# Kernel optimization log

Hardware: AMD Instinct MI355X
Metric: run time of the kernel (lower is better)

Reference implementation:

```python
import jax, jax.numpy as jnp
import numpy as np

VOCAB = 65  # 26 + 26 + 10 + 3
EMBED = 6
MAX_CTX = 8192
B, T = 4, 8192


def setup_inputs() -> dict:
    key = jax.random.key(0)
    ks = jax.random.split(key, 8)
    x = jax.random.randint(ks[0], (B, T), 0, VOCAB)
    embed_w = jax.random.normal(ks[1], (VOCAB, EMBED), dtype=jnp.float32)
    # nn.Parameter(torch.tril(torch.rand(...)))
    position_mask = jnp.tril(jax.random.uniform(ks[2], (MAX_CTX, MAX_CTX), dtype=jnp.float32))
    reset_threshold = jax.random.normal(ks[3], (1,), dtype=jnp.float32)
    temperature = jnp.sqrt(jnp.asarray(0.01, dtype=jnp.float32))
    class_transition = jax.random.normal(ks[4], (EMBED, EMBED), dtype=jnp.float32)
    reset_transition = jax.random.normal(ks[5], (EMBED, EMBED), dtype=jnp.float32)
    output = jax.random.normal(ks[6], (EMBED, VOCAB), dtype=jnp.float32)
    return {
        "x": x,
        "embed_w": embed_w,
        "position_mask": position_mask,
        "reset_threshold": reset_threshold,
        "temperature": temperature,
        "class_transition": class_transition,
        "reset_transition": reset_transition,
        "output": output,
    }


def reference(x, embed_w, position_mask, reset_threshold, temperature,
              class_transition, reset_transition, output):
    emb = embed_w[x]                               # [B,T,E]
    class_prob = jax.nn.softmax(emb, axis=-1)      # [B,T,E]
    t = x.shape[1]
    # causal pairwise similarity, weighted and reduced
    sim = jnp.einsum('bte,bse->bts', class_prob, class_prob)   # [B,T,T]
    weights = jnp.tril(position_mask[:t, :t])                  # [T,T]
    score = jnp.sum(sim * weights, axis=-1)                    # [B,T]
    score_scaled = (score - reset_threshold ** 2) / temperature ** 2
    reset = jax.nn.sigmoid(score_scaled)[..., None]            # [B,T,1]
    transition_class = class_prob @ class_transition           # [B,T,E]
    reset_class = class_prob @ reset_transition                # [B,T,E]
    next_class = reset * reset_class + (1.0 - reset) * transition_class
    return next_class @ output                                 # [B,T,V]
```

## Files before the change

### kernel.cpp

```cpp
#include <hip/hip_runtime.h>
#include <cmath>

typedef float f32x4 __attribute__((ext_vector_type(4)));

#define TT 8192
#define NV 65

__device__ __forceinline__ float dot4acc(f32x4 a, f32x4 b, float acc) {
  acc = fmaf(a[0], b[0], acc);
  acc = fmaf(a[1], b[1], acc);
  acc = fmaf(a[2], b[2], acc);
  acc = fmaf(a[3], b[3], acc);
  return acc;
}

__global__ __launch_bounds__(256) void cp_kernel(const int* __restrict__ x,
                                                 const float* __restrict__ ew,
                                                 float* __restrict__ cpt) {
  int n = blockIdx.x * 256 + threadIdx.x;
  int b = n >> 13, t = n & 8191;
  int xv = x[n];
  float v[6];
#pragma unroll
  for (int e = 0; e < 6; ++e) v[e] = ew[xv * 6 + e];
  float m = v[0];
#pragma unroll
  for (int e = 1; e < 6; ++e) m = fmaxf(m, v[e]);
  float s = 0.f;
#pragma unroll
  for (int e = 0; e < 6; ++e) { v[e] = expf(v[e] - m); s += v[e]; }
  float inv = 1.f / s;
#pragma unroll
  for (int e = 0; e < 6; ++e) cpt[(b * 6 + e) * TT + t] = v[e] * inv;
}

__global__ __launch_bounds__(256) void sticky_main(
    const float* __restrict__ W, const float* __restrict__ cpt,
    const float* __restrict__ rtp, const float* __restrict__ tp,
    const float* __restrict__ CT, const float* __restrict__ RT,
    const float* __restrict__ OM, float* __restrict__ out) {
  __shared__ __align__(16) float cp_lds[24][256];
  __shared__ __align__(16) float wsum_lds[4][4][24];
  const int j = blockIdx.x;
  const int tid = threadIdx.x;
  const int w = tid >> 6, lane = tid & 63;
  const int rbase = (w < 2) ? (8 * j + 4 * w) : (8184 - 8 * j + 4 * (w - 2));
  const int wmax = rbase + 3;
  const int k_need = 8192 - 8 * j;
  const int kl = lane * 4;

  float acc[4][24];
#pragma unroll
  for (int r = 0; r < 4; ++r)
#pragma unroll
    for (int e = 0; e < 24; ++e) acc[r][e] = 0.f;

  for (int kc = 0; kc < k_need; kc += 256) {
    __syncthreads();
#pragma unroll
    for (int i = 0; i < 6; ++i) {
      int f = tid + 256 * i;
      int e = f >> 6, c4 = (f & 63) * 4;
      *reinterpret_cast<f32x4*>(&cp_lds[e][c4]) =
          *reinterpret_cast<const f32x4*>(&cpt[e * TT + kc + c4]);
    }
    __syncthreads();
    if (kc <= wmax) {
      const float* wp = &W[(size_t)rbase * TT + kc + kl];
      f32x4 w0 = __builtin_nontemporal_load(reinterpret_cast<const f32x4*>(wp));
      f32x4 w1 = __builtin_nontemporal_load(reinterpret_cast<const f32x4*>(wp + TT));
      f32x4 w2 = __builtin_nontemporal_load(reinterpret_cast<const f32x4*>(wp + 2 * TT));
      f32x4 w3 = __builtin_nontemporal_load(reinterpret_cast<const f32x4*>(wp + 3 * TT));
#pragma unroll
      for (int e = 0; e < 24; ++e) {
        f32x4 c = *reinterpret_cast<const f32x4*>(&cp_lds[e][kl]);
        acc[0][e] = dot4acc(w0, c, acc[0][e]);
        acc[1][e] = dot4acc(w1, c, acc[1][e]);
        acc[2][e] = dot4acc(w2, c, acc[2][e]);
        acc[3][e] = dot4acc(w3, c, acc[3][e]);
      }
    }
  }

#pragma unroll
  for (int r = 0; r < 4; ++r)
#pragma unroll
    for (int e = 0; e < 24; ++e) {
      float v0 = acc[r][e];
      v0 += __shfl_xor(v0, 1);
      v0 += __shfl_xor(v0, 2);
      v0 += __shfl_xor(v0, 4);
      v0 += __shfl_xor(v0, 8);
      v0 += __shfl_xor(v0, 16);
      v0 += __shfl_xor(v0, 32);
      acc[r][e] = v0;
    }
  if (lane == 0) {
#pragma unroll
    for (int r = 0; r < 4; ++r)
#pragma unroll
      for (int g = 0; g < 6; ++g) {
        f32x4 t4;
        t4[0] = acc[r][4 * g + 0];
        t4[1] = acc[r][4 * g + 1];
        t4[2] = acc[r][4 * g + 2];
        t4[3] = acc[r][4 * g + 3];
        *reinterpret_cast<f32x4*>(&wsum_lds[w][r][4 * g]) = t4;
      }
  }
  __syncthreads();

  const int rb = lane & 15;
  const int r = rb >> 2, b = rb & 3, vi = lane >> 4;
  const int t = rbase + r;
  float cp6[6], ws6[6];
#pragma unroll
  for (int e = 0; e < 6; ++e) {
    cp6[e] = cpt[(b * 6 + e) * TT + t];
    ws6[e] = wsum_lds[w][r][b * 6 + e];
  }
  float score = 0.f;
#pragma unroll
  for (int e = 0; e < 6; ++e) score = fmaf(cp6[e], ws6[e], score);
  float rt = rtp[0];
  float temp = tp[0];
  float z = (score - rt * rt) / (temp * temp);
  float reset = 1.f / (1.f + expf(-z));
  float nc[6];
#pragma unroll
  for (int c = 0; c < 6; ++c) {
    float tc = 0.f, rc = 0.f;
#pragma unroll
    for (int e = 0; e < 6; ++e) {
      tc = fmaf(cp6[e], CT[e * 6 + c], tc);
      rc = fmaf(cp6[e], RT[e * 6 + c], rc);
    }
    nc[c] = reset * rc + (1.f - reset) * tc;
  }
  size_t obase = ((size_t)b * TT + t) * NV;
  for (int v = vi; v < NV; v += 4) {
    float o = 0.f;
#pragma unroll
    for (int c = 0; c < 6; ++c) o = fmaf(nc[c], OM[c * NV + v], o);
    out[obase + v] = o;
  }
}

extern "C" void kernel_launch(void* const* d_in, const int* in_sizes, int n_in,
                              void* d_out, int out_size, void* d_ws, size_t ws_size,
                              hipStream_t stream) {
  const int* x = (const int*)d_in[0];
  const float* ew = (const float*)d_in[1];
  const float* W = (const float*)d_in[2];
  const float* rtp = (const float*)d_in[3];
  const float* tp = (const float*)d_in[4];
  const float* CT = (const float*)d_in[5];
  const float* RT = (const float*)d_in[6];
  const float* OM = (const float*)d_in[7];
  float* out = (float*)d_out;
  float* cpt = (float*)d_ws;

  hipLaunchKernelGGL(cp_kernel, dim3(128), dim3(256), 0, stream, x, ew, cpt);
  hipLaunchKernelGGL(sticky_main, dim3(512), dim3(256), 0, stream,
                     W, cpt, rtp, tp, CT, RT, OM, out);
}
```

Baseline: 75.51 us.

## Split-K triangular tiling of weighted similarity with atomic reduction and separate epilogue

The single fused kernel, which walked k-chunks through shared memory, is replaced by a split-K kernel. It enumerates only the lower-triangular 16-row by 1024-column tiles of the position mask, each wave covering 8 rows and 12 of the 24 class columns. Class probabilities are read straight from global memory rather than staged in shared memory, which removes the per-chunk barriers. Partial sums are combined with atomicAdd into a workspace that the class-probability kernel zeroes first. A new elementwise epilogue kernel then computes the output with one thread per output element. The aims are better load balance and more bytes in flight for the large mask read, at the cost of atomics, an extra launch and redundant epilogue math.

New measurement: 113.2 us. 1.5x slower.

```diff
diff --git a/kernel.cpp b/kernel.cpp
--- a/kernel.cpp
+++ b/kernel.cpp
@@ -2,9 +2,13 @@
 #include <cmath>
 
 typedef float f32x4 __attribute__((ext_vector_type(4)));
+typedef float f32x2 __attribute__((ext_vector_type(2)));
 
 #define TT 8192
 #define NV 65
+#define KTILE 1024
+#define SUBK 256
+#define NBLK_B 2304
 
 __device__ __forceinline__ float dot4acc(f32x4 a, f32x4 b, float acc) {
   acc = fmaf(a[0], b[0], acc);
@@ -16,7 +20,8 @@
 
 __global__ __launch_bounds__(256) void cp_kernel(const int* __restrict__ x,
                                                  const float* __restrict__ ew,
-                                                 float* __restrict__ cpt) {
+                                                 float* __restrict__ cpt,
+                                                 float* __restrict__ wsum) {
   int n = blockIdx.x * 256 + threadIdx.x;
   int b = n >> 13, t = n & 8191;
   int xv = x[n];
@@ -32,92 +37,95 @@
   float inv = 1.f / s;
 #pragma unroll
   for (int e = 0; e < 6; ++e) cpt[(b * 6 + e) * TT + t] = v[e] * inv;
+  f32x2 z2 = {0.f, 0.f};
+#pragma unroll
+  for (int i = 0; i < 3; ++i)
+    *reinterpret_cast<f32x2*>(&wsum[6 * n + 2 * i]) = z2;
 }
 
-__global__ __launch_bounds__(256) void sticky_main(
-    const float* __restrict__ W, const float* __restrict__ cpt,
-    const float* __restrict__ rtp, const float* __restrict__ tp,
-    const float* __restrict__ CT, const float* __restrict__ RT,
-    const float* __restrict__ OM, float* __restrict__ out) {
-  __shared__ __align__(16) float cp_lds[24][256];
-  __shared__ __align__(16) float wsum_lds[4][4][24];
-  const int j = blockIdx.x;
+__global__ __launch_bounds__(256, 3) void sticky_B(const float* __restrict__ W,
+                                                   const float* __restrict__ cpt,
+                                                   float* __restrict__ wsum) {
+  __shared__ float ws_lds[16][24];
   const int tid = threadIdx.x;
   const int w = tid >> 6, lane = tid & 63;
-  const int rbase = (w < 2) ? (8 * j + 4 * w) : (8184 - 8 * j + 4 * (w - 2));
-  const int wmax = rbase + 3;
-  const int k_need = 8192 - 8 * j;
-  const int kl = lane * 4;
+  int bid = blockIdx.x;
+  int g = 0;
+#pragma unroll
+  for (int gg = 1; gg < 8; ++gg)
+    if (bid >= 32 * gg * (gg + 1)) g = gg;
+  int rem = bid - 32 * g * (g + 1);
+  int rt = 64 * g + rem / (g + 1);
+  int kt = rem % (g + 1);
+  const int R = rt * 16;
+  const int k0 = kt * KTILE;
+  const int rb = R + 8 * (w >> 1);
+  const int eb = 12 * (w & 1);
 
-  float acc[4][24];
+  float acc[8][12];
 #pragma unroll
-  for (int r = 0; r < 4; ++r)
+  for (int r = 0; r < 8; ++r)
 #pragma unroll
-    for (int e = 0; e < 24; ++e) acc[r][e] = 0.f;
+    for (int e2 = 0; e2 < 12; ++e2) acc[r][e2] = 0.f;
 
-  for (int kc = 0; kc < k_need; kc += 256) {
-    __syncthreads();
+#pragma unroll 1
+  for (int s = 0; s < KTILE / SUBK; ++s) {
+    const int kc = k0 + s * SUBK + lane * 4;
+    const float* wp = &W[(size_t)rb * TT + kc];
+    f32x4 wv[8];
 #pragma unroll
-    for (int i = 0; i < 6; ++i) {
-      int f = tid + 256 * i;
-      int e = f >> 6, c4 = (f & 63) * 4;
-      *reinterpret_cast<f32x4*>(&cp_lds[e][c4]) =
-          *reinterpret_cast<const f32x4*>(&cpt[e * TT + kc + c4]);
-    }
-    __syncthreads();
-    if (kc <= wmax) {
-      const float* wp = &W[(size_t)rbase * TT + kc + kl];
-      f32x4 w0 = __builtin_nontemporal_load(reinterpret_cast<const f32x4*>(wp));
-      f32x4 w1 = __builtin_nontemporal_load(reinterpret_cast<const f32x4*>(wp + TT));
-      f32x4 w2 = __builtin_nontemporal_load(reinterpret_cast<const f32x4*>(wp + 2 * TT));
-      f32x4 w3 = __builtin_nontemporal_load(reinterpret_cast<const f32x4*>(wp + 3 * TT));
+    for (int r = 0; r < 8; ++r)
+      wv[r] = __builtin_nontemporal_load(
+          reinterpret_cast<const f32x4*>(wp + (size_t)r * TT));
 #pragma unroll
-      for (int e = 0; e < 24; ++e) {
-        f32x4 c = *reinterpret_cast<const f32x4*>(&cp_lds[e][kl]);
-        acc[0][e] = dot4acc(w0, c, acc[0][e]);
-        acc[1][e] = dot4acc(w1, c, acc[1][e]);
-        acc[2][e] = dot4acc(w2, c, acc[2][e]);
-        acc[3][e] = dot4acc(w3, c, acc[3][e]);
-      }
+    for (int e2 = 0; e2 < 12; ++e2) {
+      f32x4 c = *reinterpret_cast<const f32x4*>(&cpt[(size_t)(eb + e2) * TT + kc]);
+#pragma unroll
+      for (int r = 0; r < 8; ++r) acc[r][e2] = dot4acc(wv[r], c, acc[r][e2]);
     }
   }
 
 #pragma unroll
-  for (int r = 0; r < 4; ++r)
+  for (int r = 0; r < 8; ++r)
 #pragma unroll
-    for (int e = 0; e < 24; ++e) {
-      float v0 = acc[r][e];
+    for (int e2 = 0; e2 < 12; ++e2) {
+      float v0 = acc[r][e2];
       v0 += __shfl_xor(v0, 1);
       v0 += __shfl_xor(v0, 2);
       v0 += __shfl_xor(v0, 4);
       v0 += __shfl_xor(v0, 8);
       v0 += __shfl_xor(v0, 16);
       v0 += __shfl_xor(v0, 32);
-      acc[r][e] = v0;
+      acc[r][e2] = v0;
     }
   if (lane == 0) {
 #pragma unroll
-    for (int r = 0; r < 4; ++r)
+    for (int r = 0; r < 8; ++r)
 #pragma unroll
-      for (int g = 0; g < 6; ++g) {
-        f32x4 t4;
-        t4[0] = acc[r][4 * g + 0];
-        t4[1] = acc[r][4 * g + 1];
-        t4[2] = acc[r][4 * g + 2];
-        t4[3] = acc[r][4 * g + 3];
-        *reinterpret_cast<f32x4*>(&wsum_lds[w][r][4 * g]) = t4;
-      }
+      for (int e2 = 0; e2 < 12; ++e2)
+        ws_lds[8 * (w >> 1) + r][eb + e2] = acc[r][e2];
   }
   __syncthreads();
+  for (int i = tid; i < 384; i += 256) {
+    int row = i / 24, col = i - row * 24;
+    atomicAdd(&wsum[(R + row) * 24 + col], ws_lds[row][col]);
+  }
+}
 
-  const int rb = lane & 15;
-  const int r = rb >> 2, b = rb & 3, vi = lane >> 4;
-  const int t = rbase + r;
+__global__ __launch_bounds__(256) void epi_kernel(
+    const float* __restrict__ cpt, const float* __restrict__ wsum,
+    const float* __restrict__ rtp, const float* __restrict__ tp,
+    const float* __restrict__ CT, const float* __restrict__ RT,
+    const float* __restrict__ OM, float* __restrict__ out) {
+  int n = blockIdx.x * 256 + threadIdx.x;
+  int bt = n / NV;
+  int v = n - bt * NV;
+  int b = bt >> 13, t = bt & 8191;
   float cp6[6], ws6[6];
 #pragma unroll
   for (int e = 0; e < 6; ++e) {
     cp6[e] = cpt[(b * 6 + e) * TT + t];
-    ws6[e] = wsum_lds[w][r][b * 6 + e];
+    ws6[e] = wsum[t * 24 + b * 6 + e];
   }
   float score = 0.f;
 #pragma unroll
@@ -126,7 +134,7 @@
   float temp = tp[0];
   float z = (score - rt * rt) / (temp * temp);
   float reset = 1.f / (1.f + expf(-z));
-  float nc[6];
+  float o = 0.f;
 #pragma unroll
   for (int c = 0; c < 6; ++c) {
     float tc = 0.f, rc = 0.f;
@@ -135,15 +143,10 @@
       tc = fmaf(cp6[e], CT[e * 6 + c], tc);
       rc = fmaf(cp6[e], RT[e * 6 + c], rc);
     }
-    nc[c] = reset * rc + (1.f - reset) * tc;
+    float nc = reset * rc + (1.f - reset) * tc;
+    o = fmaf(nc, OM[c * NV + v], o);
   }
-  size_t obase = ((size_t)b * TT + t) * NV;
-  for (int v = vi; v < NV; v += 4) {
-    float o = 0.f;
-#pragma unroll
-    for (int c = 0; c < 6; ++c) o = fmaf(nc[c], OM[c * NV + v], o);
-    out[obase + v] = o;
-  }
+  out[n] = o;
 }
 
 extern "C" void kernel_launch(void* const* d_in, const int* in_sizes, int n_in,
@@ -159,8 +162,11 @@
   const float* OM = (const float*)d_in[7];
   float* out = (float*)d_out;
   float* cpt = (float*)d_ws;
+  float* wsum = (float*)d_ws + 24 * TT;
 
-  hipLaunchKernelGGL(cp_kernel, dim3(128), dim3(256), 0, stream, x, ew, cpt);
-  hipLaunchKernelGGL(sticky_main, dim3(512), dim3(256), 0, stream,
-                     W, cpt, rtp, tp, CT, RT, OM, out);
+  hipLaunchKernelGGL(cp_kernel, dim3(128), dim3(256), 0, stream, x, ew, cpt, wsum);
+  hipLaunchKernelGGL(sticky_B, dim3(NBLK_B), dim3(256), 0, stream, W, cpt, wsum);
+  int nout = 4 * TT * NV;
+  hipLaunchKernelGGL(epi_kernel, dim3(nout / 256), dim3(256), 0, stream,
+                     cpt, wsum, rtp, tp, CT, RT, OM, out);
 }
```

## Balance causal row work across waves by pairing low and high rows per wave

Applied to the files above, without the earlier changes.

Before, waves 0-1 of each block owned four short (low-index) rows and sat idle for most chunks while waves 2-3 processed four long rows. Now each wave owns two low rows and two high rows, so all four waves do work in every chunk and the per-block load is even across waves. It also adds a launch-bounds occupancy hint of two blocks per CU and splits the small softmax kernel into more, smaller blocks. The trade-off is a branchier inner loop and possible register pressure from the occupancy hint.

After: 76.00 us. Within noise of the previous version (+0.6%).

```diff
diff --git a/kernel.cpp b/kernel.cpp
--- a/kernel.cpp
+++ b/kernel.cpp
@@ -14,10 +14,10 @@
   return acc;
 }
 
-__global__ __launch_bounds__(256) void cp_kernel(const int* __restrict__ x,
+__global__ __launch_bounds__(128) void cp_kernel(const int* __restrict__ x,
                                                  const float* __restrict__ ew,
                                                  float* __restrict__ cpt) {
-  int n = blockIdx.x * 256 + threadIdx.x;
+  int n = blockIdx.x * 128 + threadIdx.x;
   int b = n >> 13, t = n & 8191;
   int xv = x[n];
   float v[6];
@@ -34,20 +34,25 @@
   for (int e = 0; e < 6; ++e) cpt[(b * 6 + e) * TT + t] = v[e] * inv;
 }
 
-__global__ __launch_bounds__(256) void sticky_main(
+__global__ __launch_bounds__(256, 2) void sticky_fused(
     const float* __restrict__ W, const float* __restrict__ cpt,
     const float* __restrict__ rtp, const float* __restrict__ tp,
     const float* __restrict__ CT, const float* __restrict__ RT,
     const float* __restrict__ OM, float* __restrict__ out) {
   __shared__ __align__(16) float cp_lds[24][256];
-  __shared__ __align__(16) float wsum_lds[4][4][24];
+  __shared__ float ws_lds[4][4][24];
   const int j = blockIdx.x;
   const int tid = threadIdx.x;
   const int w = tid >> 6, lane = tid & 63;
-  const int rbase = (w < 2) ? (8 * j + 4 * w) : (8184 - 8 * j + 4 * (w - 2));
-  const int wmax = rbase + 3;
+  const int kl = lane * 4;
+  const int l0 = 8 * j + 2 * w;
+  const int h0 = 8184 - 8 * j + 2 * w;
+  const int klow_end = l0 + 2;
   const int k_need = 8192 - 8 * j;
-  const int kl = lane * 4;
+  const int nch = (k_need + 255) >> 8;
+
+  const float* wl = W + (size_t)l0 * TT;
+  const float* wh = W + (size_t)h0 * TT;
 
   float acc[4][24];
 #pragma unroll
@@ -55,7 +60,9 @@
 #pragma unroll
     for (int e = 0; e < 24; ++e) acc[r][e] = 0.f;
 
-  for (int kc = 0; kc < k_need; kc += 256) {
+#pragma unroll 1
+  for (int ch = 0; ch < nch; ++ch) {
+    const int kc = ch << 8;
     __syncthreads();
 #pragma unroll
     for (int i = 0; i < 6; ++i) {
@@ -65,19 +72,29 @@
           *reinterpret_cast<const f32x4*>(&cpt[e * TT + kc + c4]);
     }
     __syncthreads();
-    if (kc <= wmax) {
-      const float* wp = &W[(size_t)rbase * TT + kc + kl];
-      f32x4 w0 = __builtin_nontemporal_load(reinterpret_cast<const f32x4*>(wp));
-      f32x4 w1 = __builtin_nontemporal_load(reinterpret_cast<const f32x4*>(wp + TT));
-      f32x4 w2 = __builtin_nontemporal_load(reinterpret_cast<const f32x4*>(wp + 2 * TT));
-      f32x4 w3 = __builtin_nontemporal_load(reinterpret_cast<const f32x4*>(wp + 3 * TT));
+    f32x4 wh0 = __builtin_nontemporal_load(
+        reinterpret_cast<const f32x4*>(wh + kc + kl));
+    f32x4 wh1 = __builtin_nontemporal_load(
+        reinterpret_cast<const f32x4*>(wh + TT + kc + kl));
+    if (kc < klow_end) {
+      f32x4 wl0 = __builtin_nontemporal_load(
+          reinterpret_cast<const f32x4*>(wl + kc + kl));
+      f32x4 wl1 = __builtin_nontemporal_load(
+          reinterpret_cast<const f32x4*>(wl + TT + kc + kl));
 #pragma unroll
       for (int e = 0; e < 24; ++e) {
         f32x4 c = *reinterpret_cast<const f32x4*>(&cp_lds[e][kl]);
-        acc[0][e] = dot4acc(w0, c, acc[0][e]);
-        acc[1][e] = dot4acc(w1, c, acc[1][e]);
-        acc[2][e] = dot4acc(w2, c, acc[2][e]);
-        acc[3][e] = dot4acc(w3, c, acc[3][e]);
+        acc[0][e] = dot4acc(wl0, c, acc[0][e]);
+        acc[1][e] = dot4acc(wl1, c, acc[1][e]);
+        acc[2][e] = dot4acc(wh0, c, acc[2][e]);
+        acc[3][e] = dot4acc(wh1, c, acc[3][e]);
+      }
+    } else {
+#pragma unroll
+      for (int e = 0; e < 24; ++e) {
+        f32x4 c = *reinterpret_cast<const f32x4*>(&cp_lds[e][kl]);
+        acc[2][e] = dot4acc(wh0, c, acc[2][e]);
+        acc[3][e] = dot4acc(wh1, c, acc[3][e]);
       }
     }
   }
@@ -86,38 +103,31 @@
   for (int r = 0; r < 4; ++r)
 #pragma unroll
     for (int e = 0; e < 24; ++e) {
-      float v0 = acc[r][e];
-      v0 += __shfl_xor(v0, 1);
-      v0 += __shfl_xor(v0, 2);
-      v0 += __shfl_xor(v0, 4);
-      v0 += __shfl_xor(v0, 8);
-      v0 += __shfl_xor(v0, 16);
-      v0 += __shfl_xor(v0, 32);
-      acc[r][e] = v0;
+      float v = acc[r][e];
+      v += __shfl_xor(v, 1);
+      v += __shfl_xor(v, 2);
+      v += __shfl_xor(v, 4);
+      v += __shfl_xor(v, 8);
+      v += __shfl_xor(v, 16);
+      v += __shfl_xor(v, 32);
+      acc[r][e] = v;
     }
   if (lane == 0) {
 #pragma unroll
     for (int r = 0; r < 4; ++r)
 #pragma unroll
-      for (int g = 0; g < 6; ++g) {
-        f32x4 t4;
-        t4[0] = acc[r][4 * g + 0];
-        t4[1] = acc[r][4 * g + 1];
-        t4[2] = acc[r][4 * g + 2];
-        t4[3] = acc[r][4 * g + 3];
-        *reinterpret_cast<f32x4*>(&wsum_lds[w][r][4 * g]) = t4;
-      }
+      for (int e = 0; e < 24; ++e) ws_lds[w][r][e] = acc[r][e];
   }
   __syncthreads();
 
   const int rb = lane & 15;
   const int r = rb >> 2, b = rb & 3, vi = lane >> 4;
-  const int t = rbase + r;
+  const int t = (r < 2) ? (l0 + r) : (h0 + (r - 2));
   float cp6[6], ws6[6];
 #pragma unroll
   for (int e = 0; e < 6; ++e) {
     cp6[e] = cpt[(b * 6 + e) * TT + t];
-    ws6[e] = wsum_lds[w][r][b * 6 + e];
+    ws6[e] = ws_lds[w][r][b * 6 + e];
   }
   float score = 0.f;
 #pragma unroll
@@ -160,7 +170,7 @@
   float* out = (float*)d_out;
   float* cpt = (float*)d_ws;
 
-  hipLaunchKernelGGL(cp_kernel, dim3(128), dim3(256), 0, stream, x, ew, cpt);
-  hipLaunchKernelGGL(sticky_main, dim3(512), dim3(256), 0, stream,
+  hipLaunchKernelGGL(cp_kernel, dim3(256), dim3(128), 0, stream, x, ew, cpt);
+  hipLaunchKernelGGL(sticky_fused, dim3(512), dim3(256), 0, stream,
                      W, cpt, rtp, tp, CT, RT, OM, out);
 }
```
